# Performance work log

Hardware: AMD Instinct MI355X
Metric: run time of the kernel (lower is better)

The kernel has to match this reference:

```python
import jax, jax.numpy as jnp
import numpy as np

B, DIM, D_IN, HID, N_HID_EXTRA = 65536, 128, 64, 512, 2  # num_hidden_layers=3 -> 2 extra hidden linears
LOG_SCALE_CLAMP = 2.0


def _mlp(x, Win, bin_, Whid, bhid, Wout, bout):
    # torch nn.Linear: y = x @ W.T + b
    h = jax.nn.relu(x @ Win.T + bin_)
    for i in range(Whid.shape[0]):  # fixed small layer loop
        h = jax.nn.relu(h @ Whid[i].T + bhid[i])
    return h @ Wout.T + bout


def setup_inputs() -> dict:
    key = jax.random.key(0)
    ks = jax.random.split(key, 13)
    w = lambda k, shp: (jax.random.normal(k, shp, dtype=jnp.float32) * 0.05)
    d_out = DIM - D_IN
    return {
        "z": jax.random.normal(ks[0], (B, DIM), dtype=jnp.float32),
        "s_Win": w(ks[1], (HID, D_IN)),   "s_bin": jnp.zeros((HID,), jnp.float32),
        "s_Whid": w(ks[2], (N_HID_EXTRA, HID, HID)), "s_bhid": jnp.zeros((N_HID_EXTRA, HID), jnp.float32),
        "s_Wout": w(ks[3], (d_out, HID)), "s_bout": jnp.zeros((d_out,), jnp.float32),
        "t_Win": w(ks[4], (HID, D_IN)),   "t_bin": jnp.zeros((HID,), jnp.float32),
        "t_Whid": w(ks[5], (N_HID_EXTRA, HID, HID)), "t_bhid": jnp.zeros((N_HID_EXTRA, HID), jnp.float32),
        "t_Wout": w(ks[6], (d_out, HID)), "t_bout": jnp.zeros((d_out,), jnp.float32),
    }


def reference(z, s_Win, s_bin, s_Whid, s_bhid, s_Wout, s_bout,
              t_Win, t_bin, t_Whid, t_bhid, t_Wout, t_bout):
    # mask = first D_IN dims -> gather reduces to slicing
    z1 = z[:, :D_IN]   # (B, d_in)  passthrough half
    z2 = z[:, D_IN:]   # (B, d_out) transformed half
    log_s = jnp.clip(_mlp(z1, s_Win, s_bin, s_Whid, s_bhid, s_Wout, s_bout),
                     -LOG_SCALE_CLAMP, LOG_SCALE_CLAMP)
    t = _mlp(z1, t_Win, t_bin, t_Whid, t_bhid, t_Wout, t_bout)
    z2_out = z2 * jnp.exp(log_s) + t
    z_out = jnp.concatenate([z1, z2_out], axis=1)  # scatter back per mask
    log_det = log_s.sum(axis=-1)                   # (B,)
    return (z_out, log_det)
```

## Files before the change

### kernel.cpp

```cpp
#include <hip/hip_runtime.h>
#include <stdint.h>


#define NROWS 65536
#define RPB   128
#define NBLK  (NROWS / RPB)

#define OFF_S_WIN   0
#define OFF_S_WHID  32768
#define OFF_S_WOUT  557056
#define OFF_T_WIN   589824
#define OFF_T_WHID  622592
#define OFF_T_WOUT  1146880
#define W_ELEMS     1179648

typedef __attribute__((ext_vector_type(8))) short short8;
typedef __attribute__((ext_vector_type(4))) float f32x4;

__device__ __forceinline__ uint32_t f2bf1(float f) {
  uint32_t u = __float_as_uint(f);
  return (u + 0x7fffu + ((u >> 16) & 1u)) >> 16;
}
__device__ __forceinline__ uint32_t pk2bf(float a, float b) {
  return f2bf1(a) | (f2bf1(b) << 16);
}

__global__ void cvt_weights(const float* __restrict__ sWin, const float* __restrict__ sWhid,
                            const float* __restrict__ sWout, const float* __restrict__ tWin,
                            const float* __restrict__ tWhid, const float* __restrict__ tWout,
                            uint16_t* __restrict__ wbf) {
  int g = blockIdx.x * blockDim.x + threadIdx.x;
  int e = g * 4;
  if (e >= W_ELEMS) return;
  const float* src; int off;
  if      (e < OFF_S_WHID) { src = sWin;  off = e; }
  else if (e < OFF_S_WOUT) { src = sWhid; off = e - OFF_S_WHID; }
  else if (e < OFF_T_WIN)  { src = sWout; off = e - OFF_S_WOUT; }
  else if (e < OFF_T_WHID) { src = tWin;  off = e - OFF_T_WIN; }
  else if (e < OFF_T_WOUT) { src = tWhid; off = e - OFF_T_WHID; }
  else                     { src = tWout; off = e - OFF_T_WOUT; }
  f32x4 v = *(const f32x4*)(src + off);
  uint2 r; r.x = pk2bf(v.x, v.y); r.y = pk2bf(v.z, v.w);
  *(uint2*)(wbf + e) = r;
}

template<bool BF>
__device__ __forceinline__ short8 ldW(const uint16_t* __restrict__ wb,
                                      const float* __restrict__ wf, int idx) {
  if (BF) {
    return *(const short8*)(wb + idx);
  } else {
    f32x4 x = *(const f32x4*)(wf + idx);
    f32x4 y = *(const f32x4*)(wf + idx + 4);
    short8 r;
    r[0] = (short)f2bf1(x.x); r[1] = (short)f2bf1(x.y);
    r[2] = (short)f2bf1(x.z); r[3] = (short)f2bf1(x.w);
    r[4] = (short)f2bf1(y.x); r[5] = (short)f2bf1(y.y);
    r[6] = (short)f2bf1(y.z); r[7] = (short)f2bf1(y.w);
    return r;
  }
}

__device__ __forceinline__ void store_h(f32x4 acc[4][8], const float* __restrict__ bias,
                                        uint16_t* hdst, int wave, int lane) {
  const int l15 = lane & 15, lq = lane >> 4;
  __syncthreads();
  char* wp = (char*)hdst + wave * 16384 + (lq >> 1) * 2048 + (lq & 1) * 8 + l15 * 16;
  #pragma unroll
  for (int rt = 0; rt < 4; ++rt) {
    const int n0 = wave * 64 + rt * 16 + lq * 4;
    f32x4 bv = *(const f32x4*)(bias + n0);
    #pragma unroll
    for (int ct = 0; ct < 8; ++ct) {
      f32x4 v = acc[rt][ct] + bv;
      uint2 p;
      p.x = pk2bf(fmaxf(v.x, 0.f), fmaxf(v.y, 0.f));
      p.y = pk2bf(fmaxf(v.z, 0.f), fmaxf(v.w, 0.f));
      *(uint2*)(wp + rt * 4096 + ct * 256) = p;
    }
  }
  __syncthreads();
}

template<bool BF>
__device__ __forceinline__ void dense_in(
    const uint16_t* __restrict__ wb, const float* __restrict__ wf,
    const float* __restrict__ bias, const float* __restrict__ z, long rowbase,
    uint16_t* hdst, int wave, int lane) {
  const int l15 = lane & 15, lq = lane >> 4;
  f32x4 acc[4][8];
  #pragma unroll
  for (int rt = 0; rt < 4; ++rt)
    #pragma unroll
    for (int ct = 0; ct < 8; ++ct) acc[rt][ct] = (f32x4){0.f, 0.f, 0.f, 0.f};
  const int wbase = (wave * 64 + l15) * 64 + lq * 8;
  #pragma unroll
  for (int k0 = 0; k0 < 64; k0 += 32) {
    short8 a[4];
    #pragma unroll
    for (int rt = 0; rt < 4; ++rt) a[rt] = ldW<BF>(wb, wf, wbase + rt * 1024 + k0);
    #pragma unroll
    for (int ct = 0; ct < 8; ++ct) {
      const float* zp = z + (rowbase + ct * 16 + l15) * 128 + lq * 8 + k0;
      f32x4 u = *(const f32x4*)zp;
      f32x4 v = *(const f32x4*)(zp + 4);
      short8 b;
      b[0] = (short)f2bf1(u.x); b[1] = (short)f2bf1(u.y);
      b[2] = (short)f2bf1(u.z); b[3] = (short)f2bf1(u.w);
      b[4] = (short)f2bf1(v.x); b[5] = (short)f2bf1(v.y);
      b[6] = (short)f2bf1(v.z); b[7] = (short)f2bf1(v.w);
      #pragma unroll
      for (int rt = 0; rt < 4; ++rt)
        acc[rt][ct] = __builtin_amdgcn_mfma_f32_16x16x32_bf16(a[rt], b, acc[rt][ct], 0, 0, 0);
    }
  }
  store_h(acc, bias, hdst, wave, lane);
}

template<bool BF>
__device__ __forceinline__ void dense_relu512(
    const uint16_t* __restrict__ wb, const float* __restrict__ wf,
    const float* __restrict__ bias, uint16_t* hbuf, int wave, int lane) {
  const int l15 = lane & 15, lq = lane >> 4;
  f32x4 acc[4][8];
  #pragma unroll
  for (int rt = 0; rt < 4; ++rt)
    #pragma unroll
    for (int ct = 0; ct < 8; ++ct) acc[rt][ct] = (f32x4){0.f, 0.f, 0.f, 0.f};
  const int wbase = (wave * 64 + l15) * 512 + lq * 8;
  const char* bb = (const char*)hbuf + l15 * 16 + lq * 2048;

  short8 a[2][4];
  #pragma unroll
  for (int rt = 0; rt < 4; ++rt) a[0][rt] = ldW<BF>(wb, wf, wbase + rt * 8192);
  short8 bcur = *(const short8*)bb;

  #pragma unroll 1
  for (int ko = 0; ko < 512; ko += 128) {
    #pragma unroll
    for (int kk = 0; kk < 4; ++kk) {
      int kn = ko + kk * 32 + 32;
      if (kn > 480) kn = 480;
      #pragma unroll
      for (int rt = 0; rt < 4; ++rt)
        a[(kk + 1) & 1][rt] = ldW<BF>(wb, wf, wbase + rt * 8192 + kn);
      __builtin_amdgcn_s_setprio(1);
      #pragma unroll
      for (int ct = 0; ct < 8; ++ct) {
        const int noff = (ct < 7) ? (kk * 8192 + (ct + 1) * 256) : ((kk + 1) * 8192);
        short8 bn = *(const short8*)(bb + noff);
        #pragma unroll
        for (int rt = 0; rt < 4; ++rt)
          acc[rt][ct] = __builtin_amdgcn_mfma_f32_16x16x32_bf16(a[kk & 1][rt], bcur, acc[rt][ct], 0, 0, 0);
        bcur = bn;
      }
      __builtin_amdgcn_s_setprio(0);
    }
    bb += 32768;
  }
  store_h(acc, bias, hbuf, wave, lane);
}

template<bool BF>
__device__ __forceinline__ void final_layer(
    const uint16_t* __restrict__ wb, const float* __restrict__ wf,
    const uint16_t* hbuf, int wave, int lane, f32x4 acc[4][2]) {
  const int l15 = lane & 15, lq = lane >> 4;
  #pragma unroll
  for (int rt = 0; rt < 4; ++rt)
    #pragma unroll
    for (int ct = 0; ct < 2; ++ct) acc[rt][ct] = (f32x4){0.f, 0.f, 0.f, 0.f};
  const int wbase = l15 * 512 + lq * 8;
  const char* fb = (const char*)hbuf + (wave * 32 + l15) * 16 + lq * 2048;
  #pragma unroll 1
  for (int ko = 0; ko < 512; ko += 128) {
    #pragma unroll
    for (int kk = 0; kk < 4; ++kk) {
      short8 a[4];
      #pragma unroll
      for (int rt = 0; rt < 4; ++rt)
        a[rt] = ldW<BF>(wb, wf, wbase + rt * 8192 + ko + kk * 32);
      #pragma unroll
      for (int ct = 0; ct < 2; ++ct) {
        short8 b = *(const short8*)(fb + kk * 8192 + ct * 256);
        #pragma unroll
        for (int rt = 0; rt < 4; ++rt)
          acc[rt][ct] = __builtin_amdgcn_mfma_f32_16x16x32_bf16(a[rt], b, acc[rt][ct], 0, 0, 0);
      }
    }
    fb += 32768;
  }
}

template<bool BF>
__global__ __launch_bounds__(512, 2) void coupling(
    const float* __restrict__ z,
    const float* __restrict__ sWin, const float* __restrict__ sbin,
    const float* __restrict__ sWhid, const float* __restrict__ sbhid,
    const float* __restrict__ sWout, const float* __restrict__ sbout,
    const float* __restrict__ tWin, const float* __restrict__ tbin,
    const float* __restrict__ tWhid, const float* __restrict__ tbhid,
    const float* __restrict__ tWout, const float* __restrict__ tbout,
    const uint16_t* __restrict__ wbf, float* __restrict__ out) {
  extern __shared__ __align__(16) uint16_t h[];
  const int tid = threadIdx.x;
  const int wave = tid >> 6, lane = tid & 63;
  const int l15 = lane & 15, lq = lane >> 4;
  const long rowbase = (long)blockIdx.x * RPB;

  dense_in<BF>(wbf + OFF_S_WIN, sWin, sbin, z, rowbase, h, wave, lane);
  dense_relu512<BF>(wbf + OFF_S_WHID, sWhid, sbhid, h, wave, lane);
  dense_relu512<BF>(wbf + OFF_S_WHID + 262144, sWhid + 262144, sbhid + 512, h, wave, lane);

  if (wave < 4) {
    f32x4 acc[4][2];
    final_layer<BF>(wbf + OFF_S_WOUT, sWout, h, wave, lane, acc);
    #pragma unroll
    for (int ct = 0; ct < 2; ++ct) {
      const long row = rowbase + wave * 32 + ct * 16 + l15;
      float sum = 0.f;
      #pragma unroll
      for (int rt = 0; rt < 4; ++rt) {
        f32x4 bv = *(const f32x4*)(sbout + rt * 16 + lq * 4);
        f32x4 v = acc[rt][ct] + bv;
        v.x = fminf(fmaxf(v.x, -2.f), 2.f);
        v.y = fminf(fmaxf(v.y, -2.f), 2.f);
        v.z = fminf(fmaxf(v.z, -2.f), 2.f);
        v.w = fminf(fmaxf(v.w, -2.f), 2.f);
        sum += v.x + v.y + v.z + v.w;
        *(f32x4*)(out + row * 128 + 64 + rt * 16 + lq * 4) = v;
      }
      sum += __shfl_xor(sum, 16, 64);
      sum += __shfl_xor(sum, 32, 64);
      if (lane < 16) out[(long)NROWS * 128 + row] = sum;
    }
  } else {
    #pragma unroll
    for (int i = 0; i < 8; ++i) {
      int v = (wave - 4) * 64 + lane + i * 256;
      int row = v >> 4, kc = (v & 15) * 4;
      *(f32x4*)(out + (rowbase + row) * 128 + kc) =
          *(const f32x4*)(z + (rowbase + row) * 128 + kc);
    }
  }
  __syncthreads();

  dense_in<BF>(wbf + OFF_T_WIN, tWin, tbin, z, rowbase, h, wave, lane);
  dense_relu512<BF>(wbf + OFF_T_WHID, tWhid, tbhid, h, wave, lane);
  dense_relu512<BF>(wbf + OFF_T_WHID + 262144, tWhid + 262144, tbhid + 512, h, wave, lane);

  if (wave < 4) {
    f32x4 acc[4][2];
    final_layer<BF>(wbf + OFF_T_WOUT, tWout, h, wave, lane, acc);
    #pragma unroll
    for (int ct = 0; ct < 2; ++ct) {
      const long row = rowbase + wave * 32 + ct * 16 + l15;
      #pragma unroll
      for (int rt = 0; rt < 4; ++rt) {
        f32x4 bv = *(const f32x4*)(tbout + rt * 16 + lq * 4);
        f32x4 tv = acc[rt][ct] + bv;
        const long o = row * 128 + 64 + rt * 16 + lq * 4;
        f32x4 ls = *(const f32x4*)(out + o);
        f32x4 z2 = *(const f32x4*)(z + o);
        f32x4 r;
        r.x = z2.x * __expf(ls.x) + tv.x;
        r.y = z2.y * __expf(ls.y) + tv.y;
        r.z = z2.z * __expf(ls.z) + tv.z;
        r.w = z2.w * __expf(ls.w) + tv.w;
        *(f32x4*)(out + o) = r;
      }
    }
  }
}

extern "C" void kernel_launch(void* const* d_in, const int* in_sizes, int n_in,
                              void* d_out, int out_size, void* d_ws, size_t ws_size,
                              hipStream_t stream) {
  const float* z     = (const float*)d_in[0];
  const float* sWin  = (const float*)d_in[1];
  const float* sbin  = (const float*)d_in[2];
  const float* sWhid = (const float*)d_in[3];
  const float* sbhid = (const float*)d_in[4];
  const float* sWout = (const float*)d_in[5];
  const float* sbout = (const float*)d_in[6];
  const float* tWin  = (const float*)d_in[7];
  const float* tbin  = (const float*)d_in[8];
  const float* tWhid = (const float*)d_in[9];
  const float* tbhid = (const float*)d_in[10];
  const float* tWout = (const float*)d_in[11];
  const float* tbout = (const float*)d_in[12];
  float* out = (float*)d_out;
  const size_t lds_bytes = 139264;

  if (ws_size >= (size_t)W_ELEMS * sizeof(uint16_t)) {
    uint16_t* wbf = (uint16_t*)d_ws;
    cvt_weights<<<W_ELEMS / 4 / 256, 256, 0, stream>>>(sWin, sWhid, sWout, tWin, tWhid, tWout, wbf);
    coupling<true><<<NBLK, 512, lds_bytes, stream>>>(z, sWin, sbin, sWhid, sbhid, sWout, sbout,
                                                     tWin, tbin, tWhid, tbhid, tWout, tbout, wbf, out);
  } else {
    coupling<false><<<NBLK, 512, lds_bytes, stream>>>(z, sWin, sbin, sWhid, sbhid, sWout, sbout,
                                                      tWin, tbin, tWhid, tbhid, tWout, tbout,
                                                      (const uint16_t*)d_in[1], out);
  }
}
```

Measured before the change: 238.5 us.

## Switch MLP matmuls from 16x16x32 to 32x32x16 bf16 MFMA tiles

Reworks every dense layer (input, hidden, output) to use 32x32x16 bf16 MFMA instructions instead of 16x16x32. Accumulators become 16-wide vectors, and the LDS activation layout, weight indexing, epilogue store and final reductions are remapped to match. The hidden-layer loop is restructured into a double-buffered A/B ping-pong over both weight and activation fragments. The goal is fewer MFMA issues and fewer operand loads per FLOP. The trade-off is a different register footprint and LDS access pattern, which could change bank conflicts or occupancy under launch_bounds(512,2).

```diff
diff --git a/kernel.cpp b/kernel.cpp
--- a/kernel.cpp
+++ b/kernel.cpp
@@ -14,8 +14,9 @@
 #define OFF_T_WOUT  1146880
 #define W_ELEMS     1179648
 
-typedef __attribute__((ext_vector_type(8))) short short8;
-typedef __attribute__((ext_vector_type(4))) float f32x4;
+typedef __attribute__((ext_vector_type(8)))  short short8;
+typedef __attribute__((ext_vector_type(4)))  float f32x4;
+typedef __attribute__((ext_vector_type(16))) float f32x16;
 
 __device__ __forceinline__ uint32_t f2bf1(float f) {
   uint32_t u = __float_as_uint(f);
@@ -61,22 +62,28 @@
   }
 }
 
-__device__ __forceinline__ void store_h(f32x4 acc[4][8], const float* __restrict__ bias,
-                                        uint16_t* hdst, int wave, int lane) {
-  const int l15 = lane & 15, lq = lane >> 4;
+__device__ __forceinline__ void store_h32(f32x16 acc[8], const float* __restrict__ bias,
+                                          uint16_t* hdst, int wave, int lane) {
+  const int l31 = lane & 31, lh = lane >> 5;
   __syncthreads();
-  char* wp = (char*)hdst + wave * 16384 + (lq >> 1) * 2048 + (lq & 1) * 8 + l15 * 16;
-  #pragma unroll
-  for (int rt = 0; rt < 4; ++rt) {
-    const int n0 = wave * 64 + rt * 16 + lq * 4;
-    f32x4 bv = *(const f32x4*)(bias + n0);
-    #pragma unroll
-    for (int ct = 0; ct < 8; ++ct) {
-      f32x4 v = acc[rt][ct] + bv;
-      uint2 p;
-      p.x = pk2bf(fmaxf(v.x, 0.f), fmaxf(v.y, 0.f));
-      p.y = pk2bf(fmaxf(v.z, 0.f), fmaxf(v.w, 0.f));
-      *(uint2*)(wp + rt * 4096 + ct * 256) = p;
+  char* wp = (char*)hdst + wave * 16384 + l31 * 16 + lh * 8;
+  #pragma unroll
+  for (int nt = 0; nt < 2; ++nt) {
+    #pragma unroll
+    for (int q = 0; q < 4; ++q) {
+      const int m0 = wave * 64 + nt * 32 + q * 8 + lh * 4;
+      f32x4 bv = *(const f32x4*)(bias + m0);
+      #pragma unroll
+      for (int rt = 0; rt < 4; ++rt) {
+        float v0 = acc[nt * 4 + rt][q * 4 + 0] + bv.x;
+        float v1 = acc[nt * 4 + rt][q * 4 + 1] + bv.y;
+        float v2 = acc[nt * 4 + rt][q * 4 + 2] + bv.z;
+        float v3 = acc[nt * 4 + rt][q * 4 + 3] + bv.w;
+        uint2 p;
+        p.x = pk2bf(fmaxf(v0, 0.f), fmaxf(v1, 0.f));
+        p.y = pk2bf(fmaxf(v2, 0.f), fmaxf(v3, 0.f));
+        *(uint2*)(wp + nt * 8192 + q * 2048 + rt * 512) = p;
+      }
     }
   }
   __syncthreads();
@@ -87,21 +94,19 @@
     const uint16_t* __restrict__ wb, const float* __restrict__ wf,
     const float* __restrict__ bias, const float* __restrict__ z, long rowbase,
     uint16_t* hdst, int wave, int lane) {
-  const int l15 = lane & 15, lq = lane >> 4;
-  f32x4 acc[4][8];
-  #pragma unroll
-  for (int rt = 0; rt < 4; ++rt)
-    #pragma unroll
-    for (int ct = 0; ct < 8; ++ct) acc[rt][ct] = (f32x4){0.f, 0.f, 0.f, 0.f};
-  const int wbase = (wave * 64 + l15) * 64 + lq * 8;
-  #pragma unroll
-  for (int k0 = 0; k0 < 64; k0 += 32) {
-    short8 a[4];
-    #pragma unroll
-    for (int rt = 0; rt < 4; ++rt) a[rt] = ldW<BF>(wb, wf, wbase + rt * 1024 + k0);
-    #pragma unroll
-    for (int ct = 0; ct < 8; ++ct) {
-      const float* zp = z + (rowbase + ct * 16 + l15) * 128 + lq * 8 + k0;
+  const int l31 = lane & 31, lh = lane >> 5;
+  f32x16 acc[8];
+  #pragma unroll
+  for (int i = 0; i < 8; ++i) acc[i] = (f32x16)0.f;
+  const int wrow = (64 * wave + l31) * 64 + 8 * lh;
+  #pragma unroll
+  for (int ks = 0; ks < 4; ++ks) {
+    short8 a[2];
+    #pragma unroll
+    for (int nt = 0; nt < 2; ++nt) a[nt] = ldW<BF>(wb, wf, wrow + nt * 2048 + ks * 16);
+    #pragma unroll
+    for (int rt = 0; rt < 4; ++rt) {
+      const float* zp = z + (rowbase + rt * 32 + l31) * 128 + ks * 16 + 8 * lh;
       f32x4 u = *(const f32x4*)zp;
       f32x4 v = *(const f32x4*)(zp + 4);
       short8 b;
@@ -110,82 +115,90 @@
       b[4] = (short)f2bf1(v.x); b[5] = (short)f2bf1(v.y);
       b[6] = (short)f2bf1(v.z); b[7] = (short)f2bf1(v.w);
       #pragma unroll
-      for (int rt = 0; rt < 4; ++rt)
-        acc[rt][ct] = __builtin_amdgcn_mfma_f32_16x16x32_bf16(a[rt], b, acc[rt][ct], 0, 0, 0);
-    }
-  }
-  store_h(acc, bias, hdst, wave, lane);
+      for (int nt = 0; nt < 2; ++nt)
+        acc[nt * 4 + rt] = __builtin_amdgcn_mfma_f32_32x32x16_bf16(a[nt], b, acc[nt * 4 + rt], 0, 0, 0);
+    }
+  }
+  store_h32(acc, bias, hdst, wave, lane);
 }
 
 template<bool BF>
 __device__ __forceinline__ void dense_relu512(
     const uint16_t* __restrict__ wb, const float* __restrict__ wf,
     const float* __restrict__ bias, uint16_t* hbuf, int wave, int lane) {
-  const int l15 = lane & 15, lq = lane >> 4;
-  f32x4 acc[4][8];
-  #pragma unroll
-  for (int rt = 0; rt < 4; ++rt)
-    #pragma unroll
-    for (int ct = 0; ct < 8; ++ct) acc[rt][ct] = (f32x4){0.f, 0.f, 0.f, 0.f};
-  const int wbase = (wave * 64 + l15) * 512 + lq * 8;
-  const char* bb = (const char*)hbuf + l15 * 16 + lq * 2048;
-
-  short8 a[2][4];
-  #pragma unroll
-  for (int rt = 0; rt < 4; ++rt) a[0][rt] = ldW<BF>(wb, wf, wbase + rt * 8192);
-  short8 bcur = *(const short8*)bb;
+  const int l31 = lane & 31, lh = lane >> 5;
+  f32x16 acc[8];
+  #pragma unroll
+  for (int i = 0; i < 8; ++i) acc[i] = (f32x16)0.f;
+  const int wrow = (64 * wave + l31) * 512 + 8 * lh;
+  const char* bb = (const char*)hbuf + lh * 2048 + l31 * 16;
+
+  short8 aA[2], aB[2], bA[4], bB[4];
+  #pragma unroll
+  for (int nt = 0; nt < 2; ++nt) aA[nt] = ldW<BF>(wb, wf, wrow + nt * 16384);
+  #pragma unroll
+  for (int rt = 0; rt < 4; ++rt) bA[rt] = *(const short8*)(bb + rt * 512);
 
   #pragma unroll 1
-  for (int ko = 0; ko < 512; ko += 128) {
-    #pragma unroll
-    for (int kk = 0; kk < 4; ++kk) {
-      int kn = ko + kk * 32 + 32;
-      if (kn > 480) kn = 480;
-      #pragma unroll
-      for (int rt = 0; rt < 4; ++rt)
-        a[(kk + 1) & 1][rt] = ldW<BF>(wb, wf, wbase + rt * 8192 + kn);
-      __builtin_amdgcn_s_setprio(1);
-      #pragma unroll
-      for (int ct = 0; ct < 8; ++ct) {
-        const int noff = (ct < 7) ? (kk * 8192 + (ct + 1) * 256) : ((kk + 1) * 8192);
-        short8 bn = *(const short8*)(bb + noff);
+  for (int chunk = 0; chunk < 4; ++chunk) {
+    const int kbase = chunk * 128;
+    #pragma unroll
+    for (int p = 0; p < 4; ++p) {
+      {
+        const int kn = kbase + p * 32 + 16;
+        #pragma unroll
+        for (int nt = 0; nt < 2; ++nt) aB[nt] = ldW<BF>(wb, wf, wrow + nt * 16384 + kn);
         #pragma unroll
         for (int rt = 0; rt < 4; ++rt)
-          acc[rt][ct] = __builtin_amdgcn_mfma_f32_16x16x32_bf16(a[kk & 1][rt], bcur, acc[rt][ct], 0, 0, 0);
-        bcur = bn;
-      }
-      __builtin_amdgcn_s_setprio(0);
+          bB[rt] = *(const short8*)(bb + (p * 2 + 1) * 4096 + rt * 512);
+        __builtin_amdgcn_s_setprio(1);
+        #pragma unroll
+        for (int nt = 0; nt < 2; ++nt)
+          #pragma unroll
+          for (int rt = 0; rt < 4; ++rt)
+            acc[nt * 4 + rt] = __builtin_amdgcn_mfma_f32_32x32x16_bf16(aA[nt], bA[rt], acc[nt * 4 + rt], 0, 0, 0);
+        __builtin_amdgcn_s_setprio(0);
+      }
+      {
+        int kn = kbase + p * 32 + 32;
+        if (kn > 496) kn = 496;
+        #pragma unroll
+        for (int nt = 0; nt < 2; ++nt) aA[nt] = ldW<BF>(wb, wf, wrow + nt * 16384 + kn);
+        #pragma unroll
+        for (int rt = 0; rt < 4; ++rt)
+          bA[rt] = *(const short8*)(bb + (p * 2 + 2) * 4096 + rt * 512);
+        __builtin_amdgcn_s_setprio(1);
+        #pragma unroll
+        for (int nt = 0; nt < 2; ++nt)
+          #pragma unroll
+          for (int rt = 0; rt < 4; ++rt)
+            acc[nt * 4 + rt] = __builtin_amdgcn_mfma_f32_32x32x16_bf16(aB[nt], bB[rt], acc[nt * 4 + rt], 0, 0, 0);
+        __builtin_amdgcn_s_setprio(0);
+      }
     }
     bb += 32768;
   }
-  store_h(acc, bias, hbuf, wave, lane);
+  store_h32(acc, bias, hbuf, wave, lane);
 }
 
 template<bool BF>
 __device__ __forceinline__ void final_layer(
     const uint16_t* __restrict__ wb, const float* __restrict__ wf,
-    const uint16_t* hbuf, int wave, int lane, f32x4 acc[4][2]) {
-  const int l15 = lane & 15, lq = lane >> 4;
-  #pragma unroll
-  for (int rt = 0; rt < 4; ++rt)
-    #pragma unroll
-    for (int ct = 0; ct < 2; ++ct) acc[rt][ct] = (f32x4){0.f, 0.f, 0.f, 0.f};
-  const int wbase = l15 * 512 + lq * 8;
-  const char* fb = (const char*)hbuf + (wave * 32 + l15) * 16 + lq * 2048;
+    const uint16_t* hbuf, int wave, int lane, f32x16 acc[2]) {
+  const int l31 = lane & 31, lh = lane >> 5;
+  acc[0] = (f32x16)0.f; acc[1] = (f32x16)0.f;
+  const int wrow = l31 * 512 + 8 * lh;
+  const char* fb = (const char*)hbuf + lh * 2048 + l31 * 16 + wave * 512;
   #pragma unroll 1
-  for (int ko = 0; ko < 512; ko += 128) {
-    #pragma unroll
-    for (int kk = 0; kk < 4; ++kk) {
-      short8 a[4];
-      #pragma unroll
-      for (int rt = 0; rt < 4; ++rt)
-        a[rt] = ldW<BF>(wb, wf, wbase + rt * 8192 + ko + kk * 32);
-      #pragma unroll
-      for (int ct = 0; ct < 2; ++ct) {
-        short8 b = *(const short8*)(fb + kk * 8192 + ct * 256);
-        #pragma unroll
-        for (int rt = 0; rt < 4; ++rt)
-          acc[rt][ct] = __builtin_amdgcn_mfma_f32_16x16x32_bf16(a[rt], b, acc[rt][ct], 0, 0, 0);
+  for (int chunk = 0; chunk < 4; ++chunk) {
+    #pragma unroll
+    for (int p = 0; p < 8; ++p) {
+      const int k = chunk * 128 + p * 16;
+      short8 b = *(const short8*)(fb + p * 4096);
+      #pragma unroll
+      for (int nt = 0; nt < 2; ++nt) {
+        short8 a = ldW<BF>(wb, wf, wrow + nt * 16384 + k);
+        acc[nt] = __builtin_amdgcn_mfma_f32_32x32x16_bf16(a, b, acc[nt], 0, 0, 0);
       }
     }
     fb += 32768;
@@ -205,7 +218,7 @@
   extern __shared__ __align__(16) uint16_t h[];
   const int tid = threadIdx.x;
   const int wave = tid >> 6, lane = tid & 63;
-  const int l15 = lane & 15, lq = lane >> 4;
+  const int l31 = lane & 31, lh = lane >> 5;
   const long rowbase = (long)blockIdx.x * RPB;
 
   dense_in<BF>(wbf + OFF_S_WIN, sWin, sbin, z, rowbase, h, wave, lane);
@@ -213,27 +226,27 @@
   dense_relu512<BF>(wbf + OFF_S_WHID + 262144, sWhid + 262144, sbhid + 512, h, wave, lane);
 
   if (wave < 4) {
-    f32x4 acc[4][2];
+    f32x16 acc[2];
     final_layer<BF>(wbf + OFF_S_WOUT, sWout, h, wave, lane, acc);
-    #pragma unroll
-    for (int ct = 0; ct < 2; ++ct) {
-      const long row = rowbase + wave * 32 + ct * 16 + l15;
-      float sum = 0.f;
-      #pragma unroll
-      for (int rt = 0; rt < 4; ++rt) {
-        f32x4 bv = *(const f32x4*)(sbout + rt * 16 + lq * 4);
-        f32x4 v = acc[rt][ct] + bv;
-        v.x = fminf(fmaxf(v.x, -2.f), 2.f);
-        v.y = fminf(fmaxf(v.y, -2.f), 2.f);
-        v.z = fminf(fmaxf(v.z, -2.f), 2.f);
-        v.w = fminf(fmaxf(v.w, -2.f), 2.f);
+    const long row = rowbase + wave * 32 + l31;
+    float sum = 0.f;
+    #pragma unroll
+    for (int nt = 0; nt < 2; ++nt) {
+      #pragma unroll
+      for (int q = 0; q < 4; ++q) {
+        const int m0 = nt * 32 + q * 8 + lh * 4;
+        f32x4 bv = *(const f32x4*)(sbout + m0);
+        f32x4 v;
+        v.x = fminf(fmaxf(acc[nt][q * 4 + 0] + bv.x, -2.f), 2.f);
+        v.y = fminf(fmaxf(acc[nt][q * 4 + 1] + bv.y, -2.f), 2.f);
+        v.z = fminf(fmaxf(acc[nt][q * 4 + 2] + bv.z, -2.f), 2.f);
+        v.w = fminf(fmaxf(acc[nt][q * 4 + 3] + bv.w, -2.f), 2.f);
         sum += v.x + v.y + v.z + v.w;
-        *(f32x4*)(out + row * 128 + 64 + rt * 16 + lq * 4) = v;
-      }
-      sum += __shfl_xor(sum, 16, 64);
-      sum += __shfl_xor(sum, 32, 64);
-      if (lane < 16) out[(long)NROWS * 128 + row] = sum;
-    }
+        *(f32x4*)(out + row * 128 + 64 + m0) = v;
+      }
+    }
+    sum += __shfl_xor(sum, 32, 64);
+    if (lane < 32) out[(long)NROWS * 128 + row] = sum;
   } else {
     #pragma unroll
     for (int i = 0; i < 8; ++i) {
@@ -250,16 +263,21 @@
   dense_relu512<BF>(wbf + OFF_T_WHID + 262144, tWhid + 262144, tbhid + 512, h, wave, lane);
 
   if (wave < 4) {
-    f32x4 acc[4][2];
+    f32x16 acc[2];
     final_layer<BF>(wbf + OFF_T_WOUT, tWout, h, wave, lane, acc);
-    #pragma unroll
-    for (int ct = 0; ct < 2; ++ct) {
-      const long row = rowbase + wave * 32 + ct * 16 + l15;
-      #pragma unroll
-      for (int rt = 0; rt < 4; ++rt) {
-        f32x4 bv = *(const f32x4*)(tbout + rt * 16 + lq * 4);
-        f32x4 tv = acc[rt][ct] + bv;
-        const long o = row * 128 + 64 + rt * 16 + lq * 4;
+    const long row = rowbase + wave * 32 + l31;
+    #pragma unroll
+    for (int nt = 0; nt < 2; ++nt) {
+      #pragma unroll
+      for (int q = 0; q < 4; ++q) {
+        const int m0 = nt * 32 + q * 8 + lh * 4;
+        f32x4 bv = *(const f32x4*)(tbout + m0);
+        f32x4 tv;
+        tv.x = acc[nt][q * 4 + 0] + bv.x;
+        tv.y = acc[nt][q * 4 + 1] + bv.y;
+        tv.z = acc[nt][q * 4 + 2] + bv.z;
+        tv.w = acc[nt][q * 4 + 3] + bv.w;
+        const long o = row * 128 + 64 + m0;
         f32x4 ls = *(const f32x4*)(out + o);
         f32x4 z2 = *(const f32x4*)(z + o);
         f32x4 r;
```

Result: slower. 250.7 us (+5.1%).
